# Performance work log

Hardware: AMD Instinct MI355X
Metric: run time of the kernel (lower is better)

## Reference

```python
import jax, jax.numpy as jnp
import numpy as np

B, T, I, H = 4096, 128, 32, 64


def _u(key, shape, bound):
    return jax.random.uniform(key, shape, jnp.float32, -bound, bound)


def setup_inputs() -> dict:
    key = jax.random.key(0)
    ks = jax.random.split(key, 14)
    bound = 1.0 / np.sqrt(H)  # torch LSTM/Linear default init scale
    inp = {
        "x": jax.random.normal(ks[0], (B, T, I), jnp.float32),
        "Wih0": _u(ks[1], (4 * H, I), bound),
        "Whh0": _u(ks[2], (4 * H, H), bound),
        "bih0": _u(ks[3], (4 * H,), bound),
        "bhh0": _u(ks[4], (4 * H,), bound),
        "Wih1": _u(ks[5], (4 * H, H), bound),
        "Whh1": _u(ks[6], (4 * H, H), bound),
        "bih1": _u(ks[7], (4 * H,), bound),
        "bhh1": _u(ks[8], (4 * H,), bound),
        "Wc1": _u(ks[9], (32, H), 1.0 / np.sqrt(H)),
        "bc1": _u(ks[10], (32,), 1.0 / np.sqrt(H)),
        "Wc2": _u(ks[11], (1, 32), 1.0 / np.sqrt(32)),
        "bc2": _u(ks[12], (1,), 1.0 / np.sqrt(32)),
    }
    return inp


def lstm_layer(x_tbi, Wih, Whh, bih, bhh):
    """x_tbi: [T, B, in]. Returns (all hidden [T,B,H], final hidden [B,H]).
    PyTorch gate order: i, f, g, o."""
    b = x_tbi.shape[1]
    h0 = jnp.zeros((b, Whh.shape[1]), x_tbi.dtype)
    c0 = jnp.zeros_like(h0)
    # precompute input projections for all timesteps in one big GEMM
    xproj = jnp.einsum('tbi,gi->tbg', x_tbi, Wih) + (bih + bhh)

    def step(carry, xp_t):
        h, c = carry
        gates = xp_t + h @ Whh.T  # [B, 4H]
        i, f, g, o = jnp.split(gates, 4, axis=-1)
        c = jax.nn.sigmoid(f) * c + jax.nn.sigmoid(i) * jnp.tanh(g)
        h = jax.nn.sigmoid(o) * jnp.tanh(c)
        return (h, c), h

    (hT, _), hs = jax.lax.scan(step, (h0, c0), xproj)
    return hs, hT


def reference(x, Wih0, Whh0, bih0, bhh0, Wih1, Whh1, bih1, bhh1, Wc1, bc1, Wc2, bc2):
    x_tbi = jnp.transpose(x, (1, 0, 2))  # [T, B, I]
    hs0, _ = lstm_layer(x_tbi, Wih0, Whh0, bih0, bhh0)
    # dropout between layers is identity in eval mode
    _, hT = lstm_layer(hs0, Wih1, Whh1, bih1, bhh1)  # h_n[-1]: [B, H]
    hidden = jax.nn.relu(hT @ Wc1.T + bc1)  # [B, 32]; classifier dropout = identity (eval)
    out = hidden @ Wc2.T + bc2  # [B, 1]
    return out.squeeze(-1)  # [B]
```

## Files before the change

### kernel.cpp

```cpp
#include <hip/hip_runtime.h>


#define TT 128
#define II 32

typedef _Float16 half8 __attribute__((ext_vector_type(8)));
typedef float floatx4 __attribute__((ext_vector_type(4)));

#define LOG2E 1.4426950408889634f

__device__ __forceinline__ half8 cvt_frag(float4 a, float4 b) {
    half8 h;
    h[0] = (_Float16)a.x; h[1] = (_Float16)a.y; h[2] = (_Float16)a.z; h[3] = (_Float16)a.w;
    h[4] = (_Float16)b.x; h[5] = (_Float16)b.y; h[6] = (_Float16)b.z; h[7] = (_Float16)b.w;
    return h;
}

__device__ __forceinline__ half8 load_w_frag(const float* __restrict__ W, int n, int K, int k0) {
    const float* p = W + (size_t)n * K + k0;
    return cvt_frag(*(const float4*)p, *(const float4*)(p + 4));
}

__device__ __forceinline__ void lstm_cell4(const floatx4* a, float* cr, float* hnew,
                                           float nbi, float nbf, float bg2, float nbo) {
    const float nL  = -LOG2E;
    const float p2L = 2.0f * LOG2E;
    const float C43 = 30.0f * LOG2E;
    float m[4], numc[4];
    #pragma unroll
    for (int r = 0; r < 4; ++r) {
        float vf = __builtin_amdgcn_exp2f(fmaf(a[1][r], nL, nbf));
        float tg = __builtin_amdgcn_fmed3f(fmaf(a[2][r], p2L, bg2), -C43, C43);
        float u  = __builtin_amdgcn_exp2f(tg);
        float vi = __builtin_amdgcn_exp2f(fmaf(a[0][r], nL, nbi));
        float du = u + 1.0f;
        float ds = fmaf(vi, du, du);
        float df = 1.0f + vf;
        m[r]    = df * ds;
        numc[r] = fmaf(cr[r], ds, (u - 1.0f) * df);
    }
    float r01 = __builtin_amdgcn_rcpf(m[0] * m[1]);
    float r23 = __builtin_amdgcn_rcpf(m[2] * m[3]);
    float c[4];
    c[0] = numc[0] * (r01 * m[1]);
    c[1] = numc[1] * (r01 * m[0]);
    c[2] = numc[2] * (r23 * m[3]);
    c[3] = numc[3] * (r23 * m[2]);
    float dh[4], un[4];
    #pragma unroll
    for (int r = 0; r < 4; ++r) {
        cr[r] = c[r];
        float vo = __builtin_amdgcn_exp2f(fmaf(a[3][r], nL, nbo));
        float tc = __builtin_amdgcn_fmed3f(c[r] * p2L, -C43, C43);
        float uc = __builtin_amdgcn_exp2f(tc);
        float du2 = uc + 1.0f;
        dh[r] = fmaf(vo, du2, du2);
        un[r] = uc - 1.0f;
    }
    float s01 = __builtin_amdgcn_rcpf(dh[0] * dh[1]);
    float s23 = __builtin_amdgcn_rcpf(dh[2] * dh[3]);
    hnew[0] = un[0] * (s01 * dh[1]);
    hnew[1] = un[1] * (s01 * dh[0]);
    hnew[2] = un[2] * (s23 * dh[3]);
    hnew[3] = un[3] * (s23 * dh[2]);
}

__global__ __launch_bounds__(512, 2) void lstm_fused(
    const float* __restrict__ x,
    const float* __restrict__ Wih0, const float* __restrict__ Whh0,
    const float* __restrict__ bih0, const float* __restrict__ bhh0,
    const float* __restrict__ Wih1, const float* __restrict__ Whh1,
    const float* __restrict__ bih1, const float* __restrict__ bhh1,
    const float* __restrict__ Wc1, const float* __restrict__ bc1,
    const float* __restrict__ Wc2, const float* __restrict__ bc2,
    float* __restrict__ out)
{
    __shared__ __align__(16) _Float16 xs[2][16][40];
    __shared__ __align__(16) _Float16 h0s[2][16][72];
    __shared__ __align__(16) _Float16 h1s[2][16][72];
    __shared__ __align__(16) float h1f[16][68];
    __shared__ float hid[16][32];

    const int tid  = threadIdx.x;
    const int wid  = tid >> 6;
    const int w4   = wid & 3;
    const bool isL0 = (wid < 4);
    const int lane = tid & 63;
    const int q  = lane >> 4;
    const int lr = lane & 15;
    const int b0 = blockIdx.x * 16;

    const float nL  = -LOG2E;
    const float p2L = 2.0f * LOG2E;

    half8 bx0[4], bh0[4][2];
    half8 bi1[4][2], bh1[4][2];
    float bias[4];
    if (isL0) {
        #pragma unroll
        for (int g = 0; g < 4; ++g) {
            int n = (w4 + 4 * g) * 16 + lr;
            bx0[g]    = load_w_frag(Wih0, n, 32, q * 8);
            bh0[g][0] = load_w_frag(Whh0, n, 64, q * 8);
            bh0[g][1] = load_w_frag(Whh0, n, 64, 32 + q * 8);
            bias[g]   = bih0[n] + bhh0[n];
        }
    } else {
        #pragma unroll
        for (int g = 0; g < 4; ++g) {
            int n = (w4 + 4 * g) * 16 + lr;
            bi1[g][0] = load_w_frag(Wih1, n, 64, q * 8);
            bi1[g][1] = load_w_frag(Wih1, n, 64, 32 + q * 8);
            bh1[g][0] = load_w_frag(Whh1, n, 64, q * 8);
            bh1[g][1] = load_w_frag(Whh1, n, 64, 32 + q * 8);
            bias[g]   = bih1[n] + bhh1[n];
        }
    }
    const float nbi = nL * bias[0], nbf = nL * bias[1];
    const float bg2 = p2L * bias[2], nbo = nL * bias[3];
    const floatx4 zeroq = {0.f, 0.f, 0.f, 0.f};

    for (int i = tid; i < 2 * 16 * 72; i += 512) {
        ((_Float16*)h0s)[i] = (_Float16)0.0f;
        ((_Float16*)h1s)[i] = (_Float16)0.0f;
    }

    const int xm = (tid >> 4) & 15;
    const int xf = (tid & 15) * 2;
    const float* xrow = x + ((size_t)(b0 + xm) * TT) * II + xf;
    float2 xbuf = {0.f, 0.f};
    if (isL0) {
        float2 x0 = *(const float2*)(xrow);
        xs[0][xm][xf]     = (_Float16)x0.x;
        xs[0][xm][xf + 1] = (_Float16)x0.y;
        if (TT > 1) xbuf = *(const float2*)(xrow + 1 * II);
    }

    float cr[4] = {0.f, 0.f, 0.f, 0.f};

    for (int k = 0; k <= TT; ++k) {
        __syncthreads();

        const int rd = (k + 1) & 1;
        const int wr = k & 1;
        const bool doL0 = isL0 && (k < TT);
        const bool doL1 = (!isL0) && (k >= 1);
        floatx4 a[4];
        float hnew[4];
        float2 xnew = xbuf;

        if (doL0) {
            half8 xfrag = *(const half8*)&xs[wr][lr][q * 8];
            half8 h0a   = *(const half8*)&h0s[rd][lr][q * 8];
            half8 h0b   = *(const half8*)&h0s[rd][lr][32 + q * 8];
            if (k + 2 < TT) xnew = *(const float2*)(xrow + (size_t)(k + 2) * II);
            #pragma unroll
            for (int g = 0; g < 4; ++g) {
                floatx4 acc = __builtin_amdgcn_mfma_f32_16x16x32_f16(xfrag, bx0[g],    zeroq, 0, 0, 0);
                acc         = __builtin_amdgcn_mfma_f32_16x16x32_f16(h0a,   bh0[g][0], acc,   0, 0, 0);
                a[g]        = __builtin_amdgcn_mfma_f32_16x16x32_f16(h0b,   bh0[g][1], acc,   0, 0, 0);
            }
            lstm_cell4(a, cr, hnew, nbi, nbf, bg2, nbo);
        }
        if (doL1) {
            half8 g0a = *(const half8*)&h0s[rd][lr][q * 8];
            half8 g0b = *(const half8*)&h0s[rd][lr][32 + q * 8];
            half8 h1a = *(const half8*)&h1s[rd][lr][q * 8];
            half8 h1b = *(const half8*)&h1s[rd][lr][32 + q * 8];
            #pragma unroll
            for (int g = 0; g < 4; ++g) {
                floatx4 acc = __builtin_amdgcn_mfma_f32_16x16x32_f16(g0a, bi1[g][0], zeroq, 0, 0, 0);
                acc         = __builtin_amdgcn_mfma_f32_16x16x32_f16(g0b, bi1[g][1], acc,   0, 0, 0);
                acc         = __builtin_amdgcn_mfma_f32_16x16x32_f16(h1a, bh1[g][0], acc,   0, 0, 0);
                a[g]        = __builtin_amdgcn_mfma_f32_16x16x32_f16(h1b, bh1[g][1], acc,   0, 0, 0);
            }
            lstm_cell4(a, cr, hnew, nbi, nbf, bg2, nbo);
        }

        if (doL0) {
            #pragma unroll
            for (int r = 0; r < 4; ++r)
                h0s[wr][q * 4 + r][w4 * 16 + lr] = (_Float16)hnew[r];
            if (k + 1 < TT) {
                xs[rd][xm][xf]     = (_Float16)xbuf.x;
                xs[rd][xm][xf + 1] = (_Float16)xbuf.y;
            }
            xbuf = xnew;
        }
        if (doL1) {
            if (k == TT) {
                #pragma unroll
                for (int r = 0; r < 4; ++r)
                    h1f[q * 4 + r][w4 * 16 + lr] = hnew[r];
            } else {
                #pragma unroll
                for (int r = 0; r < 4; ++r)
                    h1s[wr][q * 4 + r][w4 * 16 + lr] = (_Float16)hnew[r];
            }
        }
    }
    __syncthreads();

    if (tid < 256) {
        int m = tid >> 4;
        int u = (tid & 15) * 2;
        float aa = bc1[u], bb = bc1[u + 1];
        const float* w0 = Wc1 + u * 64;
        const float* w1 = Wc1 + (u + 1) * 64;
        #pragma unroll 8
        for (int kk = 0; kk < 64; ++kk) {
            float hv = h1f[m][kk];
            aa += hv * w0[kk];
            bb += hv * w1[kk];
        }
        hid[m][u]     = fmaxf(aa, 0.f);
        hid[m][u + 1] = fmaxf(bb, 0.f);
    }
    __syncthreads();
    if (tid < 16) {
        float o = bc2[0];
        #pragma unroll
        for (int u = 0; u < 32; ++u) o += hid[tid][u] * Wc2[u];
        out[b0 + tid] = o;
    }
}

extern "C" void kernel_launch(void* const* d_in, const int* in_sizes, int n_in,
                              void* d_out, int out_size, void* d_ws, size_t ws_size,
                              hipStream_t stream) {
    (void)in_sizes; (void)n_in; (void)d_ws; (void)ws_size; (void)out_size;
    const float* x    = (const float*)d_in[0];
    const float* Wih0 = (const float*)d_in[1];
    const float* Whh0 = (const float*)d_in[2];
    const float* bih0 = (const float*)d_in[3];
    const float* bhh0 = (const float*)d_in[4];
    const float* Wih1 = (const float*)d_in[5];
    const float* Whh1 = (const float*)d_in[6];
    const float* bih1 = (const float*)d_in[7];
    const float* bhh1 = (const float*)d_in[8];
    const float* Wc1  = (const float*)d_in[9];
    const float* bc1  = (const float*)d_in[10];
    const float* Wc2  = (const float*)d_in[11];
    const float* bc2  = (const float*)d_in[12];
    lstm_fused<<<dim3(256), dim3(512), 0, stream>>>(
        x, Wih0, Whh0, bih0, bhh0, Wih1, Whh1, bih1, bhh1, Wc1, bc1, Wc2, bc2,
        (float*)d_out);
}
```

Before: 202.9 us.

## Merge layer-0 and layer-1 waves so each wave computes both LSTM layers

Halves the block from 512 to 256 threads. Each of the four waves now holds the weights for both layers and computes the layer-0 step and the layer-1 step (one timestep behind) back to back, sharing the h0 fragment reads. Prologue and epilogue steps are peeled out of the loop so no per-step branches remain. The aim is to let the MFMA chains of the two layers interleave within a wave and to cut the number of waves taking part in each barrier. The cost is more VGPR pressure per wave and half as many waves per block to hide latency.

Measured after the change: 216.4 us. 6.7% more time.

```diff
diff --git a/kernel.cpp b/kernel.cpp
--- a/kernel.cpp
+++ b/kernel.cpp
@@ -65,7 +65,7 @@
     hnew[3] = un[3] * (s23 * dh[2]);
 }
 
-__global__ __launch_bounds__(512, 2) void lstm_fused(
+__global__ __launch_bounds__(256, 1) void lstm_fused(
     const float* __restrict__ x,
     const float* __restrict__ Wih0, const float* __restrict__ Whh0,
     const float* __restrict__ bih0, const float* __restrict__ bhh0,
@@ -82,9 +82,7 @@
     __shared__ float hid[16][32];
 
     const int tid  = threadIdx.x;
-    const int wid  = tid >> 6;
-    const int w4   = wid & 3;
-    const bool isL0 = (wid < 4);
+    const int w4   = tid >> 6;
     const int lane = tid & 63;
     const int q  = lane >> 4;
     const int lr = lane & 15;
@@ -93,115 +91,132 @@
     const float nL  = -LOG2E;
     const float p2L = 2.0f * LOG2E;
 
-    half8 bx0[4], bh0[4][2];
-    half8 bi1[4][2], bh1[4][2];
-    float bias[4];
-    if (isL0) {
-        #pragma unroll
-        for (int g = 0; g < 4; ++g) {
-            int n = (w4 + 4 * g) * 16 + lr;
-            bx0[g]    = load_w_frag(Wih0, n, 32, q * 8);
-            bh0[g][0] = load_w_frag(Whh0, n, 64, q * 8);
-            bh0[g][1] = load_w_frag(Whh0, n, 64, 32 + q * 8);
-            bias[g]   = bih0[n] + bhh0[n];
-        }
-    } else {
-        #pragma unroll
-        for (int g = 0; g < 4; ++g) {
-            int n = (w4 + 4 * g) * 16 + lr;
-            bi1[g][0] = load_w_frag(Wih1, n, 64, q * 8);
-            bi1[g][1] = load_w_frag(Wih1, n, 64, 32 + q * 8);
-            bh1[g][0] = load_w_frag(Whh1, n, 64, q * 8);
-            bh1[g][1] = load_w_frag(Whh1, n, 64, 32 + q * 8);
-            bias[g]   = bih1[n] + bhh1[n];
-        }
-    }
-    const float nbi = nL * bias[0], nbf = nL * bias[1];
-    const float bg2 = p2L * bias[2], nbo = nL * bias[3];
+    half8 bx0[4], bh0[4][2], bi1[4][2], bh1[4][2];
+    float bias0[4], bias1[4];
+    #pragma unroll
+    for (int g = 0; g < 4; ++g) {
+        int n = (w4 + 4 * g) * 16 + lr;
+        bx0[g]    = load_w_frag(Wih0, n, 32, q * 8);
+        bh0[g][0] = load_w_frag(Whh0, n, 64, q * 8);
+        bh0[g][1] = load_w_frag(Whh0, n, 64, 32 + q * 8);
+        bias0[g]  = bih0[n] + bhh0[n];
+        bi1[g][0] = load_w_frag(Wih1, n, 64, q * 8);
+        bi1[g][1] = load_w_frag(Wih1, n, 64, 32 + q * 8);
+        bh1[g][0] = load_w_frag(Whh1, n, 64, q * 8);
+        bh1[g][1] = load_w_frag(Whh1, n, 64, 32 + q * 8);
+        bias1[g]  = bih1[n] + bhh1[n];
+    }
+    const float nbi0 = nL * bias0[0], nbf0 = nL * bias0[1];
+    const float bg20 = p2L * bias0[2], nbo0 = nL * bias0[3];
+    const float nbi1 = nL * bias1[0], nbf1 = nL * bias1[1];
+    const float bg21 = p2L * bias1[2], nbo1 = nL * bias1[3];
     const floatx4 zeroq = {0.f, 0.f, 0.f, 0.f};
 
-    for (int i = tid; i < 2 * 16 * 72; i += 512) {
+    for (int i = tid; i < 2 * 16 * 72; i += 256) {
         ((_Float16*)h0s)[i] = (_Float16)0.0f;
         ((_Float16*)h1s)[i] = (_Float16)0.0f;
     }
 
-    const int xm = (tid >> 4) & 15;
+    const int xm = tid >> 4;
     const int xf = (tid & 15) * 2;
     const float* xrow = x + ((size_t)(b0 + xm) * TT) * II + xf;
-    float2 xbuf = {0.f, 0.f};
-    if (isL0) {
-        float2 x0 = *(const float2*)(xrow);
-        xs[0][xm][xf]     = (_Float16)x0.x;
-        xs[0][xm][xf + 1] = (_Float16)x0.y;
-        if (TT > 1) xbuf = *(const float2*)(xrow + 1 * II);
-    }
-
-    float cr[4] = {0.f, 0.f, 0.f, 0.f};
-
-    for (int k = 0; k <= TT; ++k) {
+    float2 x0v = *(const float2*)(xrow);
+    xs[0][xm][xf]     = (_Float16)x0v.x;
+    xs[0][xm][xf + 1] = (_Float16)x0v.y;
+    float2 xbuf = *(const float2*)(xrow + II);
+
+    float cr0[4] = {0.f, 0.f, 0.f, 0.f};
+    float cr1[4] = {0.f, 0.f, 0.f, 0.f};
+    float hnew[4];
+    floatx4 a0[4], a1[4];
+
+    __syncthreads();
+
+    {
+        half8 xfrag = *(const half8*)&xs[0][lr][q * 8];
+        half8 h0a   = *(const half8*)&h0s[1][lr][q * 8];
+        half8 h0b   = *(const half8*)&h0s[1][lr][32 + q * 8];
+        float2 xnew = *(const float2*)(xrow + 2 * II);
+        #pragma unroll
+        for (int g = 0; g < 4; ++g) {
+            floatx4 acc = __builtin_amdgcn_mfma_f32_16x16x32_f16(xfrag, bx0[g],    zeroq, 0, 0, 0);
+            acc         = __builtin_amdgcn_mfma_f32_16x16x32_f16(h0a,   bh0[g][0], acc,   0, 0, 0);
+            a0[g]       = __builtin_amdgcn_mfma_f32_16x16x32_f16(h0b,   bh0[g][1], acc,   0, 0, 0);
+        }
+        lstm_cell4(a0, cr0, hnew, nbi0, nbf0, bg20, nbo0);
+        #pragma unroll
+        for (int r = 0; r < 4; ++r)
+            h0s[0][q * 4 + r][w4 * 16 + lr] = (_Float16)hnew[r];
+        xs[1][xm][xf]     = (_Float16)xbuf.x;
+        xs[1][xm][xf + 1] = (_Float16)xbuf.y;
+        xbuf = xnew;
+    }
+
+    for (int k = 1; k < TT; ++k) {
         __syncthreads();
-
         const int rd = (k + 1) & 1;
         const int wr = k & 1;
-        const bool doL0 = isL0 && (k < TT);
-        const bool doL1 = (!isL0) && (k >= 1);
-        floatx4 a[4];
-        float hnew[4];
+
+        half8 xfrag = *(const half8*)&xs[wr][lr][q * 8];
+        half8 h0a   = *(const half8*)&h0s[rd][lr][q * 8];
+        half8 h0b   = *(const half8*)&h0s[rd][lr][32 + q * 8];
+        half8 h1a   = *(const half8*)&h1s[rd][lr][q * 8];
+        half8 h1b   = *(const half8*)&h1s[rd][lr][32 + q * 8];
         float2 xnew = xbuf;
-
-        if (doL0) {
-            half8 xfrag = *(const half8*)&xs[wr][lr][q * 8];
-            half8 h0a   = *(const half8*)&h0s[rd][lr][q * 8];
-            half8 h0b   = *(const half8*)&h0s[rd][lr][32 + q * 8];
-            if (k + 2 < TT) xnew = *(const float2*)(xrow + (size_t)(k + 2) * II);
-            #pragma unroll
-            for (int g = 0; g < 4; ++g) {
-                floatx4 acc = __builtin_amdgcn_mfma_f32_16x16x32_f16(xfrag, bx0[g],    zeroq, 0, 0, 0);
-                acc         = __builtin_amdgcn_mfma_f32_16x16x32_f16(h0a,   bh0[g][0], acc,   0, 0, 0);
-                a[g]        = __builtin_amdgcn_mfma_f32_16x16x32_f16(h0b,   bh0[g][1], acc,   0, 0, 0);
-            }
-            lstm_cell4(a, cr, hnew, nbi, nbf, bg2, nbo);
-        }
-        if (doL1) {
-            half8 g0a = *(const half8*)&h0s[rd][lr][q * 8];
-            half8 g0b = *(const half8*)&h0s[rd][lr][32 + q * 8];
-            half8 h1a = *(const half8*)&h1s[rd][lr][q * 8];
-            half8 h1b = *(const half8*)&h1s[rd][lr][32 + q * 8];
-            #pragma unroll
-            for (int g = 0; g < 4; ++g) {
-                floatx4 acc = __builtin_amdgcn_mfma_f32_16x16x32_f16(g0a, bi1[g][0], zeroq, 0, 0, 0);
-                acc         = __builtin_amdgcn_mfma_f32_16x16x32_f16(g0b, bi1[g][1], acc,   0, 0, 0);
-                acc         = __builtin_amdgcn_mfma_f32_16x16x32_f16(h1a, bh1[g][0], acc,   0, 0, 0);
-                a[g]        = __builtin_amdgcn_mfma_f32_16x16x32_f16(h1b, bh1[g][1], acc,   0, 0, 0);
-            }
-            lstm_cell4(a, cr, hnew, nbi, nbf, bg2, nbo);
-        }
-
-        if (doL0) {
-            #pragma unroll
-            for (int r = 0; r < 4; ++r)
-                h0s[wr][q * 4 + r][w4 * 16 + lr] = (_Float16)hnew[r];
-            if (k + 1 < TT) {
-                xs[rd][xm][xf]     = (_Float16)xbuf.x;
-                xs[rd][xm][xf + 1] = (_Float16)xbuf.y;
-            }
-            xbuf = xnew;
-        }
-        if (doL1) {
-            if (k == TT) {
-                #pragma unroll
-                for (int r = 0; r < 4; ++r)
-                    h1f[q * 4 + r][w4 * 16 + lr] = hnew[r];
-            } else {
-                #pragma unroll
-                for (int r = 0; r < 4; ++r)
-                    h1s[wr][q * 4 + r][w4 * 16 + lr] = (_Float16)hnew[r];
-            }
-        }
+        if (k + 2 < TT) xnew = *(const float2*)(xrow + (size_t)(k + 2) * II);
+
+        #pragma unroll
+        for (int g = 0; g < 4; ++g) {
+            floatx4 acc = __builtin_amdgcn_mfma_f32_16x16x32_f16(xfrag, bx0[g],    zeroq, 0, 0, 0);
+            acc         = __builtin_amdgcn_mfma_f32_16x16x32_f16(h0a,   bh0[g][0], acc,   0, 0, 0);
+            a0[g]       = __builtin_amdgcn_mfma_f32_16x16x32_f16(h0b,   bh0[g][1], acc,   0, 0, 0);
+        }
+        #pragma unroll
+        for (int g = 0; g < 4; ++g) {
+            floatx4 acc = __builtin_amdgcn_mfma_f32_16x16x32_f16(h0a, bi1[g][0], zeroq, 0, 0, 0);
+            acc         = __builtin_amdgcn_mfma_f32_16x16x32_f16(h0b, bi1[g][1], acc,   0, 0, 0);
+            acc         = __builtin_amdgcn_mfma_f32_16x16x32_f16(h1a, bh1[g][0], acc,   0, 0, 0);
+            a1[g]       = __builtin_amdgcn_mfma_f32_16x16x32_f16(h1b, bh1[g][1], acc,   0, 0, 0);
+        }
+
+        lstm_cell4(a0, cr0, hnew, nbi0, nbf0, bg20, nbo0);
+        #pragma unroll
+        for (int r = 0; r < 4; ++r)
+            h0s[wr][q * 4 + r][w4 * 16 + lr] = (_Float16)hnew[r];
+        if (k + 1 < TT) {
+            xs[rd][xm][xf]     = (_Float16)xbuf.x;
+            xs[rd][xm][xf + 1] = (_Float16)xbuf.y;
+        }
+        xbuf = xnew;
+
+        lstm_cell4(a1, cr1, hnew, nbi1, nbf1, bg21, nbo1);
+        #pragma unroll
+        for (int r = 0; r < 4; ++r)
+            h1s[wr][q * 4 + r][w4 * 16 + lr] = (_Float16)hnew[r];
+    }
+
+    {
+        __syncthreads();
+        const int rd = (TT + 1) & 1;
+        half8 h0a = *(const half8*)&h0s[rd][lr][q * 8];
+        half8 h0b = *(const half8*)&h0s[rd][lr][32 + q * 8];
+        half8 h1a = *(const half8*)&h1s[rd][lr][q * 8];
+        half8 h1b = *(const half8*)&h1s[rd][lr][32 + q * 8];
+        #pragma unroll
+        for (int g = 0; g < 4; ++g) {
+            floatx4 acc = __builtin_amdgcn_mfma_f32_16x16x32_f16(h0a, bi1[g][0], zeroq, 0, 0, 0);
+            acc         = __builtin_amdgcn_mfma_f32_16x16x32_f16(h0b, bi1[g][1], acc,   0, 0, 0);
+            acc         = __builtin_amdgcn_mfma_f32_16x16x32_f16(h1a, bh1[g][0], acc,   0, 0, 0);
+            a1[g]       = __builtin_amdgcn_mfma_f32_16x16x32_f16(h1b, bh1[g][1], acc,   0, 0, 0);
+        }
+        lstm_cell4(a1, cr1, hnew, nbi1, nbf1, bg21, nbo1);
+        #pragma unroll
+        for (int r = 0; r < 4; ++r)
+            h1f[q * 4 + r][w4 * 16 + lr] = hnew[r];
     }
     __syncthreads();
 
-    if (tid < 256) {
+    {
         int m = tid >> 4;
         int u = (tid & 15) * 2;
         float aa = bc1[u], bb = bc1[u + 1];
@@ -242,7 +257,7 @@
     const float* bc1  = (const float*)d_in[10];
     const float* Wc2  = (const float*)d_in[11];
     const float* bc2  = (const float*)d_in[12];
-    lstm_fused<<<dim3(256), dim3(512), 0, stream>>>(
+    lstm_fused<<<dim3(256), dim3(256), 0, stream>>>(
         x, Wih0, Whh0, bih0, bhh0, Wih1, Whh1, bih1, bhh1, Wc1, bc1, Wc2, bc2,
         (float*)d_out);
 }
```
